# Kernel tuning notes

Measured on AMD Instinct MI355X. Metric: run time of the kernel, lower is better.

Reference implementation:

```python
import jax, jax.numpy as jnp
import numpy as np

IN_COUNT, OUT_COUNT, NUM_BASIS = 512, 512, 8
X_MIN, X_MAX, GAMMA_SCALE = 0.0, 1.0, 3.0
BATCH = 8192


def setup_inputs() -> dict:
    key = jax.random.key(0)
    k_x, k_c = jax.random.split(key)
    x = jax.random.uniform(k_x, (BATCH, IN_COUNT), dtype=jnp.float32)
    coeffs = 0.01 * jax.random.normal(k_c, (OUT_COUNT, IN_COUNT, NUM_BASIS), dtype=jnp.float32)
    centers_1d = jnp.linspace(X_MIN, X_MAX, NUM_BASIS, dtype=jnp.float32)
    centers = jnp.tile(centers_1d[None, :], (IN_COUNT, 1))  # (in, basis)
    delta = (X_MAX - X_MIN) / (NUM_BASIS - 1)
    gamma = GAMMA_SCALE / delta
    slopes = jnp.full((IN_COUNT, NUM_BASIS), gamma, dtype=jnp.float32)
    return {"x": x, "coeffs": coeffs, "centers": centers, "slopes": slopes}


def reference(x, coeffs, centers, slopes):
    # s_im(x) = 0.5 * (1 + tanh(gamma_im * (x_bi - c_im)))  -> (batch, in, basis)
    basis = 0.5 * (1.0 + jnp.tanh(slopes[None, :, :] * (x[:, :, None] - centers[None, :, :])))
    # y_bj = sum_{i,m} a_jim * s_bim : fused double reduction (GEMM-shaped)
    y = jnp.einsum('bim,jim->bj', basis, coeffs)
    return y
```

## Files before the change

### kernel.cpp

```cpp
#include <hip/hip_runtime.h>

#define BATCH 8192
#define INC   512
#define OUTC  512
#define NB    8
#define KDIM  (INC * NB)

#define BM 64
#define BN 128
#define BK 64
#define NKT (KDIM / BK)
#define LDA 72
#define THREADS 256

typedef __attribute__((ext_vector_type(8))) short bf16x8;
typedef __attribute__((ext_vector_type(4))) float f32x4;
typedef __attribute__((ext_vector_type(4))) int   i32x4;

static __device__ __forceinline__ unsigned int pk2(float lo, float hi) {
    return __builtin_amdgcn_perm(__builtin_bit_cast(unsigned int, hi),
                                 __builtin_bit_cast(unsigned int, lo),
                                 0x07060302u);
}

__global__ __launch_bounds__(256)
void w_prepass(const float* __restrict__ W, unsigned short* __restrict__ Wb) {
    const int base = (blockIdx.x * 256 + threadIdx.x) * 8;
    const float4 a = *(const float4*)(W + base);
    const float4 b = *(const float4*)(W + base + 4);
    const float v[8] = {a.x, a.y, a.z, a.w, b.x, b.y, b.z, b.w};
    unsigned int r[8];
#pragma unroll
    for (int i = 0; i < 8; ++i) {
        unsigned int t = __builtin_bit_cast(unsigned int, v[i]);
        t += 0x7FFFu + ((t >> 16) & 1u);
        r[i] = t >> 16;
    }
    i32x4 out = {(int)(r[0] | (r[1] << 16)), (int)(r[2] | (r[3] << 16)),
                 (int)(r[4] | (r[5] << 16)), (int)(r[6] | (r[7] << 16))};
    *(i32x4*)(Wb + base) = out;
}


template <bool DMA>
__global__ __launch_bounds__(THREADS, 2)
void tanh_basis_fused_gemm(const float* __restrict__ X,
                           const void*  __restrict__ Wsrc,
                           const float* __restrict__ CEN,
                           const float* __restrict__ SLP,
                           float* __restrict__ Y)
{
    __shared__ short As[2][BM][LDA];
    __shared__ short Bs[2][BN * BK];

    const int tid  = threadIdx.x;
    const int lane = tid & 63;
    const int wave = tid >> 6;
    const int wm   = wave & 1;
    const int wn   = wave >> 1;

    const int b0 = blockIdx.x * BM;
    const int j0 = blockIdx.y * BN;

    const float L2E = 1.4426950408889634f;
    const float g2  = 2.0f * SLP[0] * L2E;
    const float pc  = -g2;
    const float q0  = g2 * CEN[0];
    const float R   = __builtin_amdgcn_exp2f(g2 * (CEN[1] - CEN[0]));

    const int arow = tid >> 2;
    const int acol = (tid & 3) * 2;
    const float* xp = X + (size_t)(b0 + arow) * INC + acol;

    f32x4 acc[2][4];
#pragma unroll
    for (int i = 0; i < 2; ++i)
#pragma unroll
        for (int j = 0; j < 4; ++j)
            acc[i][j] = (f32x4){0.f, 0.f, 0.f, 0.f};

    const int aoff = (wm * 32 + (lane & 15)) * LDA + (lane >> 4) * 8;
    const int brow = wn * 64 + (lane & 15);
    const int low3 = lane & 7;
    const int h    = lane >> 4;
    const int boff0 = brow * BK + ((h)     ^ low3) * 8;
    const int boff1 = brow * BK + ((4 + h) ^ low3) * 8;

    const int dma_r    = lane >> 3;
    const int dma_kblk = (lane & 7) ^ dma_r;

    auto stage_B = [&](int kt, int buf) {
        if constexpr (DMA) {
            const unsigned short* Wb = (const unsigned short*)Wsrc;
#pragma unroll
            for (int q = 0; q < 4; ++q) {
                const int cc = wave * 4 + q;
                const unsigned short* gp = Wb
                    + (size_t)(j0 + cc * 8 + dma_r) * KDIM
                    + kt * BK + dma_kblk * 8;
                __builtin_amdgcn_global_load_lds(
                    (const __attribute__((address_space(1))) void*)gp,
                    (__attribute__((address_space(3))) void*)(&Bs[buf][cc * 512]),
                    16, 0, 0);
            }
        } else {
            const float* Wf = (const float*)Wsrc;
            const int frow = tid >> 1;
            const int fkh  = tid & 1;
            const float* wp = Wf + (size_t)(j0 + frow) * KDIM + kt * BK + fkh * 32;
            float4 cv[8];
#pragma unroll
            for (int q = 0; q < 8; ++q) cv[q] = ((const float4*)wp)[q];
#pragma unroll
            for (int kb = 0; kb < 4; ++kb) {
                const int kblk = fkh * 4 + kb;
                i32x4* bw = (i32x4*)(&Bs[buf][frow * BK + ((kblk ^ (frow & 7)) * 8)]);
                *bw = (i32x4){(int)pk2(cv[2*kb].x, cv[2*kb].y),
                              (int)pk2(cv[2*kb].z, cv[2*kb].w),
                              (int)pk2(cv[2*kb+1].x, cv[2*kb+1].y),
                              (int)pk2(cv[2*kb+1].z, cv[2*kb+1].w)};
            }
        }
    };

    auto stage_A = [&](float2 xq, int buf) {
        float e = __builtin_amdgcn_exp2f(fmaf(pc, xq.x, q0));
        float s[NB];
#pragma unroll
        for (int m = 0; m < NB; ++m) {
            s[m] = __builtin_amdgcn_rcpf(1.0f + e);
            e *= R;
        }
        *(i32x4*)(&As[buf][arow][acol * 8]) =
            (i32x4){(int)pk2(s[0], s[1]), (int)pk2(s[2], s[3]),
                    (int)pk2(s[4], s[5]), (int)pk2(s[6], s[7])};

        e = __builtin_amdgcn_exp2f(fmaf(pc, xq.y, q0));
#pragma unroll
        for (int m = 0; m < NB; ++m) {
            s[m] = __builtin_amdgcn_rcpf(1.0f + e);
            e *= R;
        }
        *(i32x4*)(&As[buf][arow][(acol + 1) * 8]) =
            (i32x4){(int)pk2(s[0], s[1]), (int)pk2(s[2], s[3]),
                    (int)pk2(s[4], s[5]), (int)pk2(s[6], s[7])};
    };

    float2 xv = *(const float2*)(xp);
    stage_B(0, 0);
    stage_A(xv, 0);
    xv = *(const float2*)(xp + NB);
    __syncthreads();

    for (int kt = 0; kt < NKT; ++kt) {
        const int cb = kt & 1;
        const int nb = cb ^ 1;

        if (kt + 1 < NKT) {
            stage_B(kt + 1, nb);
            stage_A(xv, nb);
            const int ktn2 = (kt + 2 < NKT) ? (kt + 2) : (NKT - 1);
            xv = *(const float2*)(xp + ktn2 * NB);
        }

        const short* abase = &As[cb][0][0];
        const short* bbase = &Bs[cb][0];
#pragma unroll
        for (int ks = 0; ks < 2; ++ks) {
            const int boffk = ks ? boff1 : boff0;
            bf16x8 af[2], bfr[4];
#pragma unroll
            for (int mf = 0; mf < 2; ++mf)
                af[mf] = *(const bf16x8*)(abase + aoff + mf * 16 * LDA + ks * 32);
#pragma unroll
            for (int nf = 0; nf < 4; ++nf)
                bfr[nf] = *(const bf16x8*)(bbase + boffk + nf * 16 * BK);
#pragma unroll
            for (int mf = 0; mf < 2; ++mf)
#pragma unroll
                for (int nf = 0; nf < 4; ++nf)
                    acc[mf][nf] = __builtin_amdgcn_mfma_f32_16x16x32_bf16(
                        af[mf], bfr[nf], acc[mf][nf], 0, 0, 0);
        }

        __syncthreads();
    }

    const int lm = (lane >> 4) * 4;
    const int ln = lane & 15;
    const int rowb = b0 + wm * 32 + lm;
    const int colb = j0 + wn * 64 + ln;
#pragma unroll
    for (int mf = 0; mf < 2; ++mf)
#pragma unroll
        for (int nf = 0; nf < 4; ++nf)
#pragma unroll
            for (int r = 0; r < 4; ++r)
                Y[(size_t)(rowb + mf * 16 + r) * OUTC + (colb + nf * 16)] = acc[mf][nf][r];
}

extern "C" void kernel_launch(void* const* d_in, const int* in_sizes, int n_in,
                              void* d_out, int out_size, void* d_ws, size_t ws_size,
                              hipStream_t stream) {
    const float* X   = (const float*)d_in[0];
    const float* W   = (const float*)d_in[1];
    const float* CEN = (const float*)d_in[2];
    const float* SLP = (const float*)d_in[3];
    float* Y = (float*)d_out;

    static_assert(BATCH % BM == 0 && OUTC % BN == 0 && KDIM % BK == 0, "tiling");
    dim3 grid(BATCH / BM, OUTC / BN);

    const size_t WB_BYTES = (size_t)OUTC * KDIM * sizeof(unsigned short);
    if (ws_size >= WB_BYTES) {
        w_prepass<<<dim3((OUTC * KDIM) / (8 * 256)), dim3(256), 0, stream>>>(
            W, (unsigned short*)d_ws);
        tanh_basis_fused_gemm<true><<<grid, dim3(THREADS), 0, stream>>>(
            X, d_ws, CEN, SLP, Y);
    } else {
        tanh_basis_fused_gemm<false><<<grid, dim3(THREADS), 0, stream>>>(
            X, (const void*)W, CEN, SLP, Y);
    }
}
```

Baseline: 130.8 us.

## Overlap async B-tile DMA with MFMA via manual waitcnt and unrolled double-buffer

Unrolls the K loop by two so the LDS buffer indices are compile-time constants, and passes buffer pointers into the staging lambdas. Each step issues the next X load, the next B tile's global_load_lds DMA and the A basis computation, then uses an explicit s_waitcnt vmcnt(5) so only the current tile's loads must finish while the next tile's loads stay in flight. The MFMA block runs between raw s_barriers at raised wave priority, with sched_barriers to keep the compiler from reordering. In exchange it adds a second barrier per step and a redundant final-step load, and it relies on hand-counted vmcnt values that must match the exact number of outstanding loads.

```diff
diff --git a/kernel.cpp b/kernel.cpp
--- a/kernel.cpp
+++ b/kernel.cpp
@@ -89,7 +89,7 @@
     const int dma_r    = lane >> 3;
     const int dma_kblk = (lane & 7) ^ dma_r;
 
-    auto stage_B = [&](int kt, int buf) {
+    auto stage_B = [&](int kt, short* bs) {
         if constexpr (DMA) {
             const unsigned short* Wb = (const unsigned short*)Wsrc;
 #pragma unroll
@@ -100,7 +100,7 @@
                     + kt * BK + dma_kblk * 8;
                 __builtin_amdgcn_global_load_lds(
                     (const __attribute__((address_space(1))) void*)gp,
-                    (__attribute__((address_space(3))) void*)(&Bs[buf][cc * 512]),
+                    (__attribute__((address_space(3))) void*)(bs + cc * 512),
                     16, 0, 0);
             }
         } else {
@@ -114,7 +114,7 @@
 #pragma unroll
             for (int kb = 0; kb < 4; ++kb) {
                 const int kblk = fkh * 4 + kb;
-                i32x4* bw = (i32x4*)(&Bs[buf][frow * BK + ((kblk ^ (frow & 7)) * 8)]);
+                i32x4* bw = (i32x4*)(bs + frow * BK + ((kblk ^ (frow & 7)) * 8));
                 *bw = (i32x4){(int)pk2(cv[2*kb].x, cv[2*kb].y),
                               (int)pk2(cv[2*kb].z, cv[2*kb].w),
                               (int)pk2(cv[2*kb+1].x, cv[2*kb+1].y),
@@ -123,7 +123,7 @@
         }
     };
 
-    auto stage_A = [&](float2 xq, int buf) {
+    auto stage_A = [&](float2 xq, short* as_base) {
         float e = __builtin_amdgcn_exp2f(fmaf(pc, xq.x, q0));
         float s[NB];
 #pragma unroll
@@ -131,7 +131,7 @@
             s[m] = __builtin_amdgcn_rcpf(1.0f + e);
             e *= R;
         }
-        *(i32x4*)(&As[buf][arow][acol * 8]) =
+        *(i32x4*)(as_base + arow * LDA + acol * 8) =
             (i32x4){(int)pk2(s[0], s[1]), (int)pk2(s[2], s[3]),
                     (int)pk2(s[4], s[5]), (int)pk2(s[6], s[7])};
 
@@ -141,30 +141,12 @@
             s[m] = __builtin_amdgcn_rcpf(1.0f + e);
             e *= R;
         }
-        *(i32x4*)(&As[buf][arow][(acol + 1) * 8]) =
+        *(i32x4*)(as_base + arow * LDA + (acol + 1) * 8) =
             (i32x4){(int)pk2(s[0], s[1]), (int)pk2(s[2], s[3]),
                     (int)pk2(s[4], s[5]), (int)pk2(s[6], s[7])};
     };
 
-    float2 xv = *(const float2*)(xp);
-    stage_B(0, 0);
-    stage_A(xv, 0);
-    xv = *(const float2*)(xp + NB);
-    __syncthreads();
-
-    for (int kt = 0; kt < NKT; ++kt) {
-        const int cb = kt & 1;
-        const int nb = cb ^ 1;
-
-        if (kt + 1 < NKT) {
-            stage_B(kt + 1, nb);
-            stage_A(xv, nb);
-            const int ktn2 = (kt + 2 < NKT) ? (kt + 2) : (NKT - 1);
-            xv = *(const float2*)(xp + ktn2 * NB);
-        }
-
-        const short* abase = &As[cb][0][0];
-        const short* bbase = &Bs[cb][0];
+    auto mfma_tile = [&](const short* abase, const short* bbase) {
 #pragma unroll
         for (int ks = 0; ks < 2; ++ks) {
             const int boffk = ks ? boff1 : boff0;
@@ -182,9 +164,42 @@
                     acc[mf][nf] = __builtin_amdgcn_mfma_f32_16x16x32_bf16(
                         af[mf], bfr[nf], acc[mf][nf], 0, 0, 0);
         }
-
-        __syncthreads();
-    }
+    };
+
+    float2 xv = *(const float2*)(xp);
+    float2 xn = *(const float2*)(xp + NB);
+    stage_B(0, &Bs[0][0]);
+    stage_A(xv, &As[0][0][0]);
+    xv = xn;
+
+#define STEP(KT, CUR, NXT)                                                   \
+    {                                                                        \
+        const int kt_ = (KT);                                                \
+        const int kx_ = (kt_ + 2 < NKT) ? kt_ + 2 : NKT - 1;                 \
+        const int kb_ = (kt_ + 1 < NKT) ? kt_ + 1 : NKT - 1;                 \
+        xn = *(const float2*)(xp + kx_ * NB);                                \
+        stage_B(kb_, &Bs[NXT][0]);                                           \
+        stage_A(xv, &As[NXT][0][0]);                                         \
+        __builtin_amdgcn_sched_barrier(0);                                   \
+        asm volatile("s_waitcnt vmcnt(5) lgkmcnt(0)" ::: "memory");          \
+        __builtin_amdgcn_s_barrier();                                        \
+        __builtin_amdgcn_sched_barrier(0);                                   \
+        __builtin_amdgcn_s_setprio(1);                                       \
+        mfma_tile(&As[CUR][0][0], &Bs[CUR][0]);                              \
+        __builtin_amdgcn_s_setprio(0);                                       \
+        __builtin_amdgcn_sched_barrier(0);                                   \
+        __builtin_amdgcn_s_barrier();                                        \
+        __builtin_amdgcn_sched_barrier(0);                                   \
+        xv = xn;                                                             \
+    }
+
+    for (int kt2 = 0; kt2 < NKT; kt2 += 2) {
+        STEP(kt2,     0, 1);
+        STEP(kt2 + 1, 1, 0);
+    }
+#undef STEP
+
+    asm volatile("s_waitcnt vmcnt(0) lgkmcnt(0)" ::: "memory");
 
     const int lm = (lane >> 4) * 4;
     const int ln = lane & 15;
```

Result: faster. 122.9 us (-6.1%).

## Double M tile to 128 and restructure pipelined main loop with unrolled steps

Applied to the files above, without the earlier changes.

Raises the batch tile from 64 to 128 rows, so each wave now computes a 64x64 output block with 16 accumulators, and each thread builds four basis vectors per k-step from a float4 load. The main loop is unrolled by two with constant buffer indices. Fragment loads are issued first, then the next A tile is generated, then the MFMAs run, so the sigmoid work can overlap the matrix-core work. The aim is more reuse of each B tile and fewer redundant W reads. In exchange, occupancy drops to one block per SIMD group (launch bounds 1) and register pressure rises. The last iteration also redundantly restages the final k tile.

```diff
diff --git a/kernel.cpp b/kernel.cpp
--- a/kernel.cpp
+++ b/kernel.cpp
@@ -6,7 +6,7 @@
 #define NB    8
 #define KDIM  (INC * NB)
 
-#define BM 64
+#define BM 128
 #define BN 128
 #define BK 64
 #define NKT (KDIM / BK)
@@ -43,7 +43,7 @@
 
 
 template <bool DMA>
-__global__ __launch_bounds__(THREADS, 2)
+__global__ __launch_bounds__(THREADS, 1)
 void tanh_basis_fused_gemm(const float* __restrict__ X,
                            const void*  __restrict__ Wsrc,
                            const float* __restrict__ CEN,
@@ -68,18 +68,18 @@
     const float q0  = g2 * CEN[0];
     const float R   = __builtin_amdgcn_exp2f(g2 * (CEN[1] - CEN[0]));
 
-    const int arow = tid >> 2;
-    const int acol = (tid & 3) * 2;
+    const int arow = tid >> 1;
+    const int acol = (tid & 1) * 4;
     const float* xp = X + (size_t)(b0 + arow) * INC + acol;
 
-    f32x4 acc[2][4];
-#pragma unroll
-    for (int i = 0; i < 2; ++i)
+    f32x4 acc[4][4];
+#pragma unroll
+    for (int i = 0; i < 4; ++i)
 #pragma unroll
         for (int j = 0; j < 4; ++j)
             acc[i][j] = (f32x4){0.f, 0.f, 0.f, 0.f};
 
-    const int aoff = (wm * 32 + (lane & 15)) * LDA + (lane >> 4) * 8;
+    const int aoff = (wm * 64 + (lane & 15)) * LDA + (lane >> 4) * 8;
     const int brow = wn * 64 + (lane & 15);
     const int low3 = lane & 7;
     const int h    = lane >> 4;
@@ -89,7 +89,7 @@
     const int dma_r    = lane >> 3;
     const int dma_kblk = (lane & 7) ^ dma_r;
 
-    auto stage_B = [&](int kt, int buf) {
+    auto stage_B = [&](int kt, short* bs) {
         if constexpr (DMA) {
             const unsigned short* Wb = (const unsigned short*)Wsrc;
 #pragma unroll
@@ -100,7 +100,7 @@
                     + kt * BK + dma_kblk * 8;
                 __builtin_amdgcn_global_load_lds(
                     (const __attribute__((address_space(1))) void*)gp,
-                    (__attribute__((address_space(3))) void*)(&Bs[buf][cc * 512]),
+                    (__attribute__((address_space(3))) void*)(bs + cc * 512),
                     16, 0, 0);
             }
         } else {
@@ -114,7 +114,7 @@
 #pragma unroll
             for (int kb = 0; kb < 4; ++kb) {
                 const int kblk = fkh * 4 + kb;
-                i32x4* bw = (i32x4*)(&Bs[buf][frow * BK + ((kblk ^ (frow & 7)) * 8)]);
+                i32x4* bw = (i32x4*)(bs + frow * BK + ((kblk ^ (frow & 7)) * 8));
                 *bw = (i32x4){(int)pk2(cv[2*kb].x, cv[2*kb].y),
                               (int)pk2(cv[2*kb].z, cv[2*kb].w),
                               (int)pk2(cv[2*kb+1].x, cv[2*kb+1].y),
@@ -123,75 +123,68 @@
         }
     };
 
-    auto stage_A = [&](float2 xq, int buf) {
-        float e = __builtin_amdgcn_exp2f(fmaf(pc, xq.x, q0));
-        float s[NB];
-#pragma unroll
-        for (int m = 0; m < NB; ++m) {
-            s[m] = __builtin_amdgcn_rcpf(1.0f + e);
-            e *= R;
+    auto stage_A = [&](float4 xq, short* as_base) {
+        const float xs[4] = {xq.x, xq.y, xq.z, xq.w};
+        short* ap = as_base + arow * LDA + acol * 8;
+#pragma unroll
+        for (int q = 0; q < 4; ++q) {
+            float e = __builtin_amdgcn_exp2f(fmaf(pc, xs[q], q0));
+            float s[NB];
+#pragma unroll
+            for (int m = 0; m < NB; ++m) {
+                s[m] = __builtin_amdgcn_rcpf(1.0f + e);
+                e *= R;
+            }
+            *(i32x4*)(ap + q * 8) =
+                (i32x4){(int)pk2(s[0], s[1]), (int)pk2(s[2], s[3]),
+                        (int)pk2(s[4], s[5]), (int)pk2(s[6], s[7])};
         }
-        *(i32x4*)(&As[buf][arow][acol * 8]) =
-            (i32x4){(int)pk2(s[0], s[1]), (int)pk2(s[2], s[3]),
-                    (int)pk2(s[4], s[5]), (int)pk2(s[6], s[7])};
-
-        e = __builtin_amdgcn_exp2f(fmaf(pc, xq.y, q0));
-#pragma unroll
-        for (int m = 0; m < NB; ++m) {
-            s[m] = __builtin_amdgcn_rcpf(1.0f + e);
-            e *= R;
-        }
-        *(i32x4*)(&As[buf][arow][(acol + 1) * 8]) =
-            (i32x4){(int)pk2(s[0], s[1]), (int)pk2(s[2], s[3]),
-                    (int)pk2(s[4], s[5]), (int)pk2(s[6], s[7])};
     };
 
-    float2 xv = *(const float2*)(xp);
-    stage_B(0, 0);
-    stage_A(xv, 0);
-    xv = *(const float2*)(xp + NB);
+    float4 xv4 = *(const float4*)(xp);
+    stage_B(0, &Bs[0][0]);
+    stage_A(xv4, &As[0][0][0]);
+    xv4 = *(const float4*)(xp + NB);
     __syncthreads();
 
-    for (int kt = 0; kt < NKT; ++kt) {
-        const int cb = kt & 1;
-        const int nb = cb ^ 1;
-
-        if (kt + 1 < NKT) {
-            stage_B(kt + 1, nb);
-            stage_A(xv, nb);
-            const int ktn2 = (kt + 2 < NKT) ? (kt + 2) : (NKT - 1);
-            xv = *(const float2*)(xp + ktn2 * NB);
-        }
-
-        const short* abase = &As[cb][0][0];
-        const short* bbase = &Bs[cb][0];
-#pragma unroll
-        for (int ks = 0; ks < 2; ++ks) {
-            const int boffk = ks ? boff1 : boff0;
-            bf16x8 af[2], bfr[4];
-#pragma unroll
-            for (int mf = 0; mf < 2; ++mf)
-                af[mf] = *(const bf16x8*)(abase + aoff + mf * 16 * LDA + ks * 32);
-#pragma unroll
-            for (int nf = 0; nf < 4; ++nf)
-                bfr[nf] = *(const bf16x8*)(bbase + boffk + nf * 16 * BK);
-#pragma unroll
-            for (int mf = 0; mf < 2; ++mf)
-#pragma unroll
-                for (int nf = 0; nf < 4; ++nf)
-                    acc[mf][nf] = __builtin_amdgcn_mfma_f32_16x16x32_bf16(
-                        af[mf], bfr[nf], acc[mf][nf], 0, 0, 0);
-        }
-
-        __syncthreads();
-    }
+#define STEP(KT, CUR, NXT)                                                     \
+    {                                                                          \
+        const int kb_ = ((KT) + 1 < NKT) ? (KT) + 1 : NKT - 1;                 \
+        const int kx_ = ((KT) + 2 < NKT) ? (KT) + 2 : NKT - 1;                 \
+        stage_B(kb_, &Bs[NXT][0]);                                             \
+        const short* abase = &As[CUR][0][0];                                   \
+        const short* bbase = &Bs[CUR][0];                                      \
+        bf16x8 af[2][4], bfr[2][4];                                            \
+        _Pragma("unroll") for (int ks = 0; ks < 2; ++ks) {                     \
+            _Pragma("unroll") for (int mf = 0; mf < 4; ++mf)                   \
+                af[ks][mf] = *(const bf16x8*)(abase + aoff + mf * 16 * LDA     \
+                                              + ks * 32);                      \
+            const int boffk = ks ? boff1 : boff0;                              \
+            _Pragma("unroll") for (int nf = 0; nf < 4; ++nf)                   \
+                bfr[ks][nf] = *(const bf16x8*)(bbase + boffk + nf * 16 * BK);  \
+        }                                                                      \
+        stage_A(xv4, &As[NXT][0][0]);          \
+        xv4 = *(const float4*)(xp + kx_ * NB);                                 \
+        _Pragma("unroll") for (int ks = 0; ks < 2; ++ks)                       \
+            _Pragma("unroll") for (int mf = 0; mf < 4; ++mf)                   \
+                _Pragma("unroll") for (int nf = 0; nf < 4; ++nf)               \
+                    acc[mf][nf] = __builtin_amdgcn_mfma_f32_16x16x32_bf16(     \
+                        af[ks][mf], bfr[ks][nf], acc[mf][nf], 0, 0, 0);        \
+        __syncthreads();                                                       \
+    }
+
+    for (int kt2 = 0; kt2 < NKT; kt2 += 2) {
+        STEP(kt2,     0, 1);
+        STEP(kt2 + 1, 1, 0);
+    }
+#undef STEP
 
     const int lm = (lane >> 4) * 4;
     const int ln = lane & 15;
-    const int rowb = b0 + wm * 32 + lm;
+    const int rowb = b0 + wm * 64 + lm;
     const int colb = j0 + wn * 64 + ln;
 #pragma unroll
-    for (int mf = 0; mf < 2; ++mf)
+    for (int mf = 0; mf < 4; ++mf)
 #pragma unroll
         for (int nf = 0; nf < 4; ++nf)
 #pragma unroll
```

After: 144.1 us. 1.1x slower.
